# Performance work log

Measured on AMD Instinct MI355X. Metric: run time of the kernel, lower is better.

Reference implementation:

```python
import jax, jax.numpy as jnp
import numpy as np
import math

D_MODEL = 1024
N_HEADS = 16
HEAD_DIM = D_MODEL // N_HEADS
B, T = 2, 2048


def _rope(q, k):
    # q, k: (B, H, T, Dh)
    Dh = q.shape[-1]
    Tq = q.shape[2]
    dim = jnp.arange(0, Dh, 2, dtype=jnp.float32)
    inv_freq = 1.0 / (10000.0 ** (dim / Dh))
    pos = jnp.arange(Tq, dtype=jnp.float32)
    freqs = pos[:, None] * inv_freq[None, :]          # (T, Dh/2)
    sin = jnp.sin(freqs)[None, None]                  # (1,1,T,Dh/2)
    cos = jnp.cos(freqs)[None, None]

    def rot(t):
        te, to = t[..., ::2], t[..., 1::2]
        re = te * cos - to * sin
        ro = te * sin + to * cos
        return jnp.stack([re, ro], axis=-1).reshape(t.shape)

    return rot(q), rot(k)


def setup_inputs() -> dict:
    key = jax.random.key(0)
    ks = jax.random.split(key, 4)
    std = 1.0 / math.sqrt(D_MODEL)
    x = jax.random.normal(ks[0], (B, T, D_MODEL), dtype=jnp.float32)
    W_qkv = jax.random.normal(ks[1], (D_MODEL, 3 * D_MODEL), dtype=jnp.float32) * std
    b_qkv = jnp.zeros((3 * D_MODEL,), dtype=jnp.float32)
    W_out = jax.random.normal(ks[2], (D_MODEL, D_MODEL), dtype=jnp.float32) * std
    b_out = jnp.zeros((D_MODEL,), dtype=jnp.float32)
    attention_mask = jnp.ones((B, T), dtype=jnp.int32)
    return {"x": x, "attention_mask": attention_mask, "W_qkv": W_qkv,
            "b_qkv": b_qkv, "W_out": W_out, "b_out": b_out}


def reference(x, attention_mask, W_qkv, b_qkv, W_out, b_out):
    Bx, Tx, D = x.shape
    qkv = x @ W_qkv + b_qkv                            # (B,T,3D)
    q, k, v = jnp.split(qkv, 3, axis=-1)
    # (B,T,H,Dh) -> (B,H,T,Dh)
    q = q.reshape(Bx, Tx, N_HEADS, HEAD_DIM).transpose(0, 2, 1, 3)
    k = k.reshape(Bx, Tx, N_HEADS, HEAD_DIM).transpose(0, 2, 1, 3)
    v = v.reshape(Bx, Tx, N_HEADS, HEAD_DIM).transpose(0, 2, 1, 3)
    q, k = _rope(q, k)
    scale = 1.0 / math.sqrt(float(HEAD_DIM))
    scores = jnp.einsum('bhqd,bhkd->bhqk', q, k) * scale
    causal = jnp.tril(jnp.ones((Tx, Tx), dtype=bool))[None, None]
    pad = attention_mask.astype(bool)[:, None, None, :]
    mask = causal & pad
    scores = jnp.where(mask, scores, -jnp.inf)
    probs = jax.nn.softmax(scores, axis=-1)
    out = jnp.einsum('bhqk,bhkd->bhqd', probs, v)      # (B,H,T,Dh)
    out = out.transpose(0, 2, 1, 3).reshape(Bx, Tx, D)
    return out @ W_out + b_out
```

## Files before the change

kernel.cpp:

```cpp
#include <hip/hip_runtime.h>
#include <math.h>
#include <stdint.h>

#define D_MODEL 1024
#define N_HEADS 16
#define HEAD_DIM 64
#define BATCH 2
#define SEQ 2048
#define TOKENS (BATCH * SEQ)

typedef __attribute__((ext_vector_type(8))) short short8;
typedef __attribute__((ext_vector_type(8))) _Float16 half8;
typedef __attribute__((ext_vector_type(4))) float floatx4;

#define BMFMA(a, b, c) __builtin_amdgcn_mfma_f32_16x16x32_bf16(a, b, c, 0, 0, 0)
#define HMFMA(a, b, c) __builtin_amdgcn_mfma_f32_16x16x32_f16(a, b, c, 0, 0, 0)

__device__ __forceinline__ unsigned short f2bf(float f) {
    uint32_t u = __float_as_uint(f);
    u += 0x7fffu + ((u >> 16) & 1u);
    return (unsigned short)(u >> 16);
}
__device__ __forceinline__ float bf2f(unsigned short h) {
    return __uint_as_float(((uint32_t)h) << 16);
}
__device__ __forceinline__ unsigned short f2h(float f) {
    union { _Float16 h; unsigned short u; } cv;
    cv.h = (_Float16)f;
    return cv.u;
}
__device__ __forceinline__ float h2f(unsigned short u) {
    union { unsigned short u; _Float16 h; } cv;
    cv.u = u;
    return (float)cv.h;
}

#define GLD_LDS16(gp, lp) __builtin_amdgcn_global_load_lds(                 \
    (const __attribute__((address_space(1))) void*)(gp),                    \
    (__attribute__((address_space(3))) void*)(lp), 16, 0, 0)

__global__ __launch_bounds__(256) void split_inputs(
    const float* __restrict__ X, const float* __restrict__ Wqkv,
    const float* __restrict__ Wout, const int* __restrict__ am,
    unsigned short* __restrict__ Axh, unsigned short* __restrict__ Bt,
    unsigned short* __restrict__ Bt2, unsigned long long* __restrict__ mbits,
    float2* __restrict__ tab)
{
    __shared__ float t[32][33];
    const int tid = threadIdx.x;
    const int bid = blockIdx.x;
    if (bid < 2048) {
        const int idx = bid * 2048 + tid * 8;
        const int row = idx >> 10;
        const int c = idx & 1023;
        float4 v0 = *(const float4*)(X + (size_t)row * 1024 + c);
        float4 v1 = *(const float4*)(X + (size_t)row * 1024 + c + 4);
        float f[8] = {v0.x, v0.y, v0.z, v0.w, v1.x, v1.y, v1.z, v1.w};
        uint32_t p[4];
#pragma unroll
        for (int j = 0; j < 4; ++j)
            p[j] = (uint32_t)f2h(f[2 * j]) | ((uint32_t)f2h(f[2 * j + 1]) << 16);
        *(uint4*)(Axh + (size_t)row * 1024 + c) = *(uint4*)p;
    } else if (bid < 5120) {
        const int id = bid - 2048;
        const int n0 = (id % 96) * 32, k0 = (id / 96) * 32;
        const int c = tid & 31, r = tid >> 5;
#pragma unroll
        for (int i = 0; i < 4; ++i)
            t[r + 8 * i][c] = Wqkv[(size_t)(k0 + r + 8 * i) * 3072 + n0 + c];
        __syncthreads();
#pragma unroll
        for (int i = 0; i < 4; ++i) {
            int dn = r + 8 * i;
            Bt[(size_t)(n0 + dn) * 1024 + k0 + c] = f2h(t[c][dn]);
        }
    } else if (bid < 6144) {
        const int id = bid - 5120;
        const int n0 = (id & 31) * 32, k0 = (id >> 5) * 32;
        const int c = tid & 31, r = tid >> 5;
#pragma unroll
        for (int i = 0; i < 4; ++i)
            t[r + 8 * i][c] = Wout[(size_t)(k0 + r + 8 * i) * 1024 + n0 + c];
        __syncthreads();
#pragma unroll
        for (int i = 0; i < 4; ++i) {
            int dn = r + 8 * i;
            Bt2[(size_t)(n0 + dn) * 1024 + k0 + c] = f2h(t[c][dn]);
        }
    } else if (bid == 6144) {
        if (tid < 64) {
            const int* a = am + tid * 64;
            unsigned long long m = 0ull;
            for (int j = 0; j < 64; ++j)
                m |= (unsigned long long)(a[j] != 0 ? 1u : 0u) << j;
            mbits[tid] = m;
        }
    } else {
        const int i = bid - 6145;
#pragma unroll
        for (int e = 0; e < 16; ++e) {
            int idx = i * 4096 + e * 256 + tid;
            int tt = idx >> 5, pr = idx & 31;
            double ex = (double)(2 * pr) / 64.0;
            float inv = (float)exp2(-ex * 13.287712379549449);
            float ang = (float)tt * inv;
            float s, c;
            __sincosf(ang, &s, &c);
            tab[idx] = make_float2(c, s);
        }
    }
}

__global__ __launch_bounds__(256) void gemm_qkv_fused(
    const unsigned short* __restrict__ Axh, const unsigned short* __restrict__ Bt,
    const float* __restrict__ bias, const float2* __restrict__ tab,
    unsigned short* __restrict__ Qh, unsigned short* __restrict__ Kh,
    unsigned short* __restrict__ Vh)
{
    __shared__ __align__(16) unsigned short sA0[4096], sA1[4096];
    __shared__ __align__(16) unsigned short sB0[4096], sB1[4096];

    const int tid = threadIdx.x;
    const int w = tid >> 6, lane = tid & 63;
    const int l15 = lane & 15, quad = lane >> 4;
    const int wm = w >> 1, wn = w & 1;

    const int lin = blockIdx.x;
    const int s = lin & 7;
    const int loc = lin >> 3;
    const int m0 = ((s >> 1) * 8 + loc / 12) * 128;
    const int n0 = ((s & 1) * 12 + loc % 12) * 128;

    const int ch = (lane & 3) ^ ((lane >> 3) & 3);
    const int sw = (quad ^ ((l15 >> 1) & 3)) * 8;

    const unsigned short* aG[2];
    const unsigned short* bG[2];
#pragma unroll
    for (int i = 0; i < 2; ++i) {
        aG[i] = Axh + (size_t)(m0 + (w * 2 + i) * 16 + (lane >> 2)) * 1024 + ch * 8;
        bG[i] = Bt + (size_t)(n0 + (w * 2 + i) * 16 + (lane >> 2)) * 1024 + ch * 8;
    }

    floatx4 acc[4][4];
#pragma unroll
    for (int fm = 0; fm < 4; ++fm)
#pragma unroll
        for (int fn = 0; fn < 4; ++fn) acc[fm][fn] = (floatx4)0.f;

    for (int ks = 0; ks < 16; ++ks) {
        const int ko = ks * 64;
        __syncthreads();
#pragma unroll
        for (int i = 0; i < 2; ++i) {
            GLD_LDS16(aG[i] + ko,      sA0 + (w * 2 + i) * 512);
            GLD_LDS16(aG[i] + ko + 32, sA1 + (w * 2 + i) * 512);
            GLD_LDS16(bG[i] + ko,      sB0 + (w * 2 + i) * 512);
            GLD_LDS16(bG[i] + ko + 32, sB1 + (w * 2 + i) * 512);
        }
        __syncthreads();

        half8 a0[4], a1[4], b0[4], b1[4];
#pragma unroll
        for (int fm = 0; fm < 4; ++fm) {
            const int off = ((wm * 4 + fm) * 16 + l15) * 32 + sw;
            a0[fm] = *(const half8*)&sA0[off];
            a1[fm] = *(const half8*)&sA1[off];
        }
#pragma unroll
        for (int fn = 0; fn < 4; ++fn) {
            const int off = ((wn * 4 + fn) * 16 + l15) * 32 + sw;
            b0[fn] = *(const half8*)&sB0[off];
            b1[fn] = *(const half8*)&sB1[off];
        }
#pragma unroll
        for (int fm = 0; fm < 4; ++fm)
#pragma unroll
            for (int fn = 0; fn < 4; ++fn) {
                floatx4 a = acc[fm][fn];
                a = HMFMA(a0[fm], b0[fn], a);
                a = HMFMA(a1[fm], b1[fn], a);
                acc[fm][fn] = a;
            }
    }

    if (n0 < 2048) {
        const bool isQ = (n0 < 1024);
        unsigned short* dst = isQ ? Qh : Kh;
        const float qs = isQ ? 0.125f : 1.0f;
#pragma unroll
        for (int fm = 0; fm < 4; ++fm)
#pragma unroll
            for (int fn = 0; fn < 4; ++fn) {
                const int col = n0 + (wn * 4 + fn) * 16 + l15;
                const int hcol = col & 1023;
                const int hh = hcol >> 6, d = hcol & 63;
                const int pr = d >> 1;
                const bool odd = (d & 1) != 0;
                const float bv = bias[col];
#pragma unroll
                for (int r = 0; r < 4; ++r) {
                    const int row = m0 + (wm * 4 + fm) * 16 + quad * 4 + r;
                    const int tg = row & 2047, bb = row >> 11;
                    float val = acc[fm][fn][r] + bv;
                    float part = __shfl_xor(val, 1);
                    const float2 cs = tab[tg * 32 + pr];
                    float res = odd ? (part * cs.y + val * cs.x)
                                    : (val * cs.x - part * cs.y);
                    dst[((size_t)(bb * 16 + hh) * SEQ + tg) * 64 + d] =
                        f2h(res * qs);
                }
            }
    } else {
#pragma unroll
        for (int fm = 0; fm < 4; ++fm)
#pragma unroll
            for (int fn = 0; fn < 4; ++fn) {
                const int col = n0 + (wn * 4 + fn) * 16 + l15;
                const int hcol = col & 1023;
                const int hh = hcol >> 6, d = hcol & 63;
                const float bv = bias[col];
                const int row0 = m0 + (wm * 4 + fm) * 16 + quad * 4;
                const int tg0 = row0 & 2047, bb = row0 >> 11;
                uint32_t pk0 = (uint32_t)f2bf(acc[fm][fn][0] + bv)
                             | ((uint32_t)f2bf(acc[fm][fn][1] + bv) << 16);
                uint32_t pk1 = (uint32_t)f2bf(acc[fm][fn][2] + bv)
                             | ((uint32_t)f2bf(acc[fm][fn][3] + bv) << 16);
                *(uint2*)(Vh + ((size_t)(bb * 16 + hh) * 64 + d) * SEQ + tg0) =
                    make_uint2(pk0, pk1);
            }
    }
}

template<int WM, int WN, int FM, int FN>
__global__ __launch_bounds__(256) void gemm_mfma_h(
    const unsigned short* __restrict__ A, int lda,
    const unsigned short* __restrict__ Bt, int ldb,
    const float* __restrict__ bias, float* __restrict__ C, int ldc,
    int mPerSlab, int nTilesN)
{
    constexpr int BM = WM * FM * 16;
    constexpr int BN = WN * FN * 16;
    constexpr int NA = BM / 64;
    constexpr int NB = BN / 64;

    __shared__ __align__(16) unsigned short sA0[BM * 32];
    __shared__ __align__(16) unsigned short sA1[BM * 32];
    __shared__ __align__(16) unsigned short sB0[BN * 32];
    __shared__ __align__(16) unsigned short sB1[BN * 32];

    const int tid = threadIdx.x;
    const int w = tid >> 6, lane = tid & 63;
    const int l15 = lane & 15, quad = lane >> 4;
    const int wm = w / WN, wn = w % WN;

    const int lin = blockIdx.x;
    const int s = lin & 7, loc = lin >> 3;
    const int m0 = (s * mPerSlab + loc / nTilesN) * BM;
    const int n0 = (loc % nTilesN) * BN;

    const int ch = (lane & 3) ^ ((lane >> 3) & 3);
    const int sw = (quad ^ ((l15 >> 1) & 3)) * 8;

    const unsigned short* aG[NA];
    const unsigned short* bG[NB];
#pragma unroll
    for (int i = 0; i < NA; ++i)
        aG[i] = A + (size_t)(m0 + (w * NA + i) * 16 + (lane >> 2)) * lda + ch * 8;
#pragma unroll
    for (int i = 0; i < NB; ++i)
        bG[i] = Bt + (size_t)(n0 + (w * NB + i) * 16 + (lane >> 2)) * ldb + ch * 8;

    floatx4 acc[FM][FN];
#pragma unroll
    for (int fm = 0; fm < FM; ++fm)
#pragma unroll
        for (int fn = 0; fn < FN; ++fn) acc[fm][fn] = (floatx4)0.f;

    for (int ks = 0; ks < 16; ++ks) {
        const int ko = ks * 64;
        __syncthreads();
#pragma unroll
        for (int i = 0; i < NA; ++i) {
            GLD_LDS16(aG[i] + ko,      sA0 + (w * NA + i) * 512);
            GLD_LDS16(aG[i] + ko + 32, sA1 + (w * NA + i) * 512);
        }
#pragma unroll
        for (int i = 0; i < NB; ++i) {
            GLD_LDS16(bG[i] + ko,      sB0 + (w * NB + i) * 512);
            GLD_LDS16(bG[i] + ko + 32, sB1 + (w * NB + i) * 512);
        }
        __syncthreads();

        half8 a0[FM], a1[FM], b0[FN], b1[FN];
#pragma unroll
        for (int fm = 0; fm < FM; ++fm) {
            const int off = ((wm * FM + fm) * 16 + l15) * 32 + sw;
            a0[fm] = *(const half8*)&sA0[off];
            a1[fm] = *(const half8*)&sA1[off];
        }
#pragma unroll
        for (int fn = 0; fn < FN; ++fn) {
            const int off = ((wn * FN + fn) * 16 + l15) * 32 + sw;
            b0[fn] = *(const half8*)&sB0[off];
            b1[fn] = *(const half8*)&sB1[off];
        }
#pragma unroll
        for (int fm = 0; fm < FM; ++fm)
#pragma unroll
            for (int fn = 0; fn < FN; ++fn) {
                floatx4 a = acc[fm][fn];
                a = HMFMA(a0[fm], b0[fn], a);
                a = HMFMA(a1[fm], b1[fn], a);
                acc[fm][fn] = a;
            }
    }

#pragma unroll
    for (int fm = 0; fm < FM; ++fm)
#pragma unroll
        for (int fn = 0; fn < FN; ++fn) {
            int col = n0 + (wn * FN + fn) * 16 + l15;
            float bv = bias[col];
#pragma unroll
            for (int r = 0; r < 4; ++r) {
                int row = m0 + (wm * FM + fm) * 16 + quad * 4 + r;
                C[(size_t)row * ldc + col] = acc[fm][fn][r] + bv;
            }
        }
}

__global__ __launch_bounds__(256, 6) void flash_mfma(
    const unsigned short* __restrict__ Qh, const unsigned short* __restrict__ Kh,
    const unsigned short* __restrict__ Vh,
    const unsigned long long* __restrict__ mbits,
    unsigned short* __restrict__ attnx,
    float* __restrict__ Opart, float* __restrict__ lpart)
{
    __shared__ __align__(16) unsigned short sK[4096];
    __shared__ __align__(16) unsigned short sV[4096];
    __shared__ __align__(16) unsigned short sP[4096];

    const int tid = threadIdx.x;
    const int lane = tid & 63, w = tid >> 6;
    const int l15 = lane & 15, quad = lane >> 4;
    const int lin0 = blockIdx.x;
    const int xcd = lin0 & 7, idx = lin0 >> 3;
    const int bh = xcd * 4 + (idx & 3);
    const int rank = idx >> 2;
    int qt, k0, kend, mode;
    if (rank < 16)        { qt = 16 + rank; k0 = 0;  kend = 15; mode = 1; }
    else {
        const int i = (rank - 16) >> 1;
        if ((rank & 1) == 0) { qt = 31 - i; k0 = 16; kend = qt; mode = 2; }
        else                 { qt = 15 - i; k0 = 0;  kend = qt; mode = 0; }
    }
    const int b = bh >> 4, h = bh & 15;
    const int sw = (quad ^ ((l15 >> 1) & 3)) * 8;
    const int ch = (lane & 3) ^ ((lane >> 3) & 3);
    unsigned short* pbase = sP + w * 1024;

    short8 ones;
#pragma unroll
    for (int jj = 0; jj < 8; ++jj) ones[jj] = (short)0x3F80;

    const size_t qb = ((size_t)bh * SEQ + qt * 64 + w * 16 + l15) * 64 + quad * 8;
    const half8 qh0 = *(const half8*)(Qh + qb);
    const half8 qh1 = *(const half8*)(Qh + qb + 32);

    unsigned int mlo = 0xffffffffu, mhi = 0xffffffffu;
    if (lane < 32) {
        unsigned long long mw = mbits[b * 32 + lane];
        mlo = (unsigned int)mw;
        mhi = (unsigned int)(mw >> 32);
    }
    const bool fullmask =
        (__ballot((mlo & mhi) == 0xffffffffu) == ~0ull);

    const size_t kRow0 = ((size_t)bh * SEQ + w * 16 + (lane >> 2)) * 64 + ch * 8;
    const size_t vRow  = ((size_t)bh * 64 + w * 16 + (lane >> 2)) * SEQ + ch * 8;

    floatx4 O[4];
    floatx4 lAcc = (floatx4)0.f;
#pragma unroll
    for (int nf = 0; nf < 4; ++nf) O[nf] = (floatx4)0.f;

    const int mg = qt * 64 + w * 16 + l15;

    for (int kt = k0; kt <= kend; ++kt) {
        __syncthreads();
        {
            const size_t kg = kRow0 + (size_t)kt * 64 * 64;
            const size_t vg = vRow + (size_t)kt * 64;
            GLD_LDS16(Kh + kg,      sK + w * 512);
            GLD_LDS16(Kh + kg + 32, sK + 2048 + w * 512);
            GLD_LDS16(Vh + vg,      sV + w * 512);
            GLD_LDS16(Vh + vg + 32, sV + 2048 + w * 512);
        }
        __syncthreads();

        const bool diag = (kt == qt);
        unsigned int wlo = 0xffffffffu, whi = 0xffffffffu;
        if (!fullmask) {
            wlo = (unsigned int)__shfl((int)mlo, kt);
            whi = (unsigned int)__shfl((int)mhi, kt);
        }

#pragma unroll
        for (int nf = 0; nf < 4; ++nf) {
            const int base = (nf * 16 + l15) * 32 + sw;
            const half8 k0v = *(const half8*)&sK[base];
            const half8 k1v = *(const half8*)&sK[2048 + base];
            floatx4 s = (floatx4)0.f;
            s = HMFMA(k0v, qh0, s);
            s = HMFMA(k1v, qh1, s);

            float pv[4];
            if (fullmask && !diag) {
#pragma unroll
                for (int r = 0; r < 4; ++r)
                    pv[r] = __expf(s[r] - 16.0f);
            } else {
                const int tb = kt * 64 + nf * 16 + quad * 4;
                const unsigned int msel = (nf & 2) ? whi : wlo;
                const int p4 = (nf & 1) * 16 + quad * 4;
#pragma unroll
                for (int r = 0; r < 4; ++r) {
                    bool ok = ((msel >> (p4 + r)) & 1u) != 0u;
                    if (diag) ok = ok && (tb + r <= mg);
                    pv[r] = ok ? __expf(s[r] - 16.0f) : 0.0f;
                }
            }
            uint32_t w0, w1;
            asm("v_cvt_pk_bf16_f32 %0, %1, %2" : "=v"(w0) : "v"(pv[0]), "v"(pv[1]));
            asm("v_cvt_pk_bf16_f32 %0, %1, %2" : "=v"(w1) : "v"(pv[2]), "v"(pv[3]));
            const int pos = (((nf & 1) * 2 + (quad >> 1)) ^ ((l15 >> 1) & 3));
            *(uint2*)(pbase + (nf >> 1) * 512 + l15 * 32 + pos * 8
                      + (quad & 1) * 4) = make_uint2(w0, w1);
        }

        const short8 pf0 = *(const short8*)(pbase + l15 * 32 + sw);
        const short8 pf1 = *(const short8*)(pbase + 512 + l15 * 32 + sw);

        lAcc = BMFMA(pf0, ones, lAcc);
        lAcc = BMFMA(pf1, ones, lAcc);
#pragma unroll
        for (int nf = 0; nf < 4; ++nf) {
            const int vb = (nf * 16 + l15) * 32 + sw;
            floatx4 o = O[nf];
            o = BMFMA(pf0, *(const short8*)&sV[vb], o);
            o = BMFMA(pf1, *(const short8*)&sV[2048 + vb], o);
            O[nf] = o;
        }
    }

    if (mode == 0) {
        float rl[4];
#pragma unroll
        for (int r = 0; r < 4; ++r) rl[r] = 1.0f / lAcc[r];
#pragma unroll
        for (int nf = 0; nf < 4; ++nf)
#pragma unroll
            for (int r = 0; r < 4; ++r) {
                const int tok = b * SEQ + qt * 64 + w * 16 + quad * 4 + r;
                const int col = h * 64 + nf * 16 + l15;
                attnx[(size_t)tok * 1024 + col] = f2h(O[nf][r] * rl[r]);
            }
    } else {
        const int qt16 = qt - 16;
        float* Op = Opart + ((mode == 2) ? 2097152 : 0)
                  + (((size_t)bh * 16 + qt16) * 64) * 64;
#pragma unroll
        for (int nf = 0; nf < 4; ++nf)
#pragma unroll
            for (int r = 0; r < 4; ++r)
                Op[(w * 16 + quad * 4 + r) * 64 + nf * 16 + l15] = O[nf][r];
        if (l15 == 0) {
            float* lp = lpart + ((mode == 2) ? 32768 : 0)
                      + (bh * 16 + qt16) * 64;
#pragma unroll
            for (int r = 0; r < 4; ++r)
                lp[w * 16 + quad * 4 + r] = lAcc[r];
        }
    }
}

__global__ __launch_bounds__(256) void flash_merge(
    const float* __restrict__ Opart, const float* __restrict__ lpart,
    unsigned short* __restrict__ attnx)
{
    const int bh = blockIdx.x >> 4, qt16 = blockIdx.x & 15;
    const int b = bh >> 4, h = bh & 15;
    const int tid = threadIdx.x;
    const int q = tid >> 2, dblk = (tid & 3) * 16;
    const size_t ob = (((size_t)bh * 16 + qt16) * 64 + q) * 64 + dblk;
    const int lb = (bh * 16 + qt16) * 64 + q;
    const float rl = 1.0f / (lpart[lb] + lpart[lb + 32768]);

    uint32_t ph[8];
#pragma unroll
    for (int i = 0; i < 4; ++i) {
        float4 a = *(const float4*)(Opart + ob + 4 * i);
        float4 c = *(const float4*)(Opart + ob + 2097152 + 4 * i);
        float f0 = (a.x + c.x) * rl, f1 = (a.y + c.y) * rl;
        float f2 = (a.z + c.z) * rl, f3 = (a.w + c.w) * rl;
        ph[2 * i]     = (uint32_t)f2h(f0) | ((uint32_t)f2h(f1) << 16);
        ph[2 * i + 1] = (uint32_t)f2h(f2) | ((uint32_t)f2h(f3) << 16);
    }
    const int tok = b * SEQ + (16 + qt16) * 64 + q;
    unsigned short* dst = attnx + (size_t)tok * 1024 + h * 64 + dblk;
    *(uint4*)dst = *(uint4*)&ph[0];
    *(uint4*)(dst + 8) = *(uint4*)&ph[4];
}

extern "C" void kernel_launch(void* const* d_in, const int* in_sizes, int n_in,
                              void* d_out, int out_size, void* d_ws, size_t ws_size,
                              hipStream_t stream)
{
    const float* x    = (const float*)d_in[0];
    const int*   am   = (const int*)d_in[1];
    const float* Wqkv = (const float*)d_in[2];
    const float* bqkv = (const float*)d_in[3];
    const float* Wout = (const float*)d_in[4];
    const float* bout = (const float*)d_in[5];
    float* out = (float*)d_out;

    char* ws = (char*)d_ws;
    unsigned short* Bt  = (unsigned short*)ws;
    unsigned short* Bt2 = (unsigned short*)(ws + 6291456);
    float2* tab = (float2*)(ws + 8388608);
    unsigned long long* mbits = (unsigned long long*)(ws + 8912896);
    unsigned short* attnx = (unsigned short*)(ws + 12582912);
    unsigned short* Qh = (unsigned short*)(ws + 62914560);
    unsigned short* Kh = (unsigned short*)(ws + 71303168);
    unsigned short* Vh = (unsigned short*)(ws + 79691776);
    unsigned short* Axh = (unsigned short*)(ws + 88080384);
    float* Opart = (float*)(ws + 88080384);
    float* lpart = (float*)(ws + 104857600);

    split_inputs<<<6161, 256, 0, stream>>>(x, Wqkv, Wout, am,
                                           Axh, Bt, Bt2, mbits, tab);

    gemm_qkv_fused<<<768, 256, 0, stream>>>(Axh, Bt, bqkv, tab, Qh, Kh, Vh);

    flash_mfma<<<1536, 256, 0, stream>>>(Qh, Kh, Vh, mbits, attnx,
                                         Opart, lpart);
    flash_merge<<<512, 256, 0, stream>>>(Opart, lpart, attnx);

    gemm_mfma_h<2, 2, 4, 4><<<256, 256, 0, stream>>>(
        attnx, 1024, Bt2, 1024, bout, out, 1024, 4, 8);
}
```

Before: 184.0 us.

## Double-buffer LDS tiles in QKV and output GEMMs to overlap loads with MFMA

```diff
diff --git a/kernel.cpp b/kernel.cpp
--- a/kernel.cpp
+++ b/kernel.cpp
@@ -38,6 +38,12 @@
 #define GLD_LDS16(gp, lp) __builtin_amdgcn_global_load_lds(                 \
     (const __attribute__((address_space(1))) void*)(gp),                    \
     (__attribute__((address_space(3))) void*)(lp), 16, 0, 0)
+
+#define PIPE_WAIT_BARRIER() do {                                            \
+    asm volatile("s_waitcnt vmcnt(0)" ::: "memory");                        \
+    __builtin_amdgcn_s_barrier();                                           \
+    __builtin_amdgcn_sched_barrier(0);                                      \
+} while (0)
 
 __global__ __launch_bounds__(256) void split_inputs(
     const float* __restrict__ X, const float* __restrict__ Wqkv,
@@ -117,8 +123,8 @@
     unsigned short* __restrict__ Qh, unsigned short* __restrict__ Kh,
     unsigned short* __restrict__ Vh)
 {
-    __shared__ __align__(16) unsigned short sA0[4096], sA1[4096];
-    __shared__ __align__(16) unsigned short sB0[4096], sB1[4096];
+    __shared__ __align__(16) unsigned short sA[2][4096];
+    __shared__ __align__(16) unsigned short sB[2][4096];
 
     const int tid = threadIdx.x;
     const int w = tid >> 6, lane = tid & 63;
@@ -148,40 +154,40 @@
 #pragma unroll
         for (int fn = 0; fn < 4; ++fn) acc[fm][fn] = (floatx4)0.f;
 
-    for (int ks = 0; ks < 16; ++ks) {
-        const int ko = ks * 64;
-        __syncthreads();
-#pragma unroll
-        for (int i = 0; i < 2; ++i) {
-            GLD_LDS16(aG[i] + ko,      sA0 + (w * 2 + i) * 512);
-            GLD_LDS16(aG[i] + ko + 32, sA1 + (w * 2 + i) * 512);
-            GLD_LDS16(bG[i] + ko,      sB0 + (w * 2 + i) * 512);
-            GLD_LDS16(bG[i] + ko + 32, sB1 + (w * 2 + i) * 512);
-        }
-        __syncthreads();
-
-        half8 a0[4], a1[4], b0[4], b1[4];
-#pragma unroll
-        for (int fm = 0; fm < 4; ++fm) {
-            const int off = ((wm * 4 + fm) * 16 + l15) * 32 + sw;
-            a0[fm] = *(const half8*)&sA0[off];
-            a1[fm] = *(const half8*)&sA1[off];
-        }
-#pragma unroll
-        for (int fn = 0; fn < 4; ++fn) {
-            const int off = ((wn * 4 + fn) * 16 + l15) * 32 + sw;
-            b0[fn] = *(const half8*)&sB0[off];
-            b1[fn] = *(const half8*)&sB1[off];
-        }
+#pragma unroll
+    for (int i = 0; i < 2; ++i) {
+        GLD_LDS16(aG[i], &sA[0][(w * 2 + i) * 512]);
+        GLD_LDS16(bG[i], &sB[0][(w * 2 + i) * 512]);
+    }
+    PIPE_WAIT_BARRIER();
+
+    int cur = 0;
+    for (int ks = 0; ks < 32; ++ks) {
+        if (ks < 31) {
+            const int ko = (ks + 1) * 32;
+#pragma unroll
+            for (int i = 0; i < 2; ++i) {
+                GLD_LDS16(aG[i] + ko, &sA[cur ^ 1][(w * 2 + i) * 512]);
+                GLD_LDS16(bG[i] + ko, &sB[cur ^ 1][(w * 2 + i) * 512]);
+            }
+        }
+        __builtin_amdgcn_sched_barrier(0);
+
+        half8 af[4], bf[4];
 #pragma unroll
         for (int fm = 0; fm < 4; ++fm)
-#pragma unroll
-            for (int fn = 0; fn < 4; ++fn) {
-                floatx4 a = acc[fm][fn];
-                a = HMFMA(a0[fm], b0[fn], a);
-                a = HMFMA(a1[fm], b1[fn], a);
-                acc[fm][fn] = a;
-            }
+            af[fm] = *(const half8*)&sA[cur][((wm * 4 + fm) * 16 + l15) * 32 + sw];
+#pragma unroll
+        for (int fn = 0; fn < 4; ++fn)
+            bf[fn] = *(const half8*)&sB[cur][((wn * 4 + fn) * 16 + l15) * 32 + sw];
+#pragma unroll
+        for (int fm = 0; fm < 4; ++fm)
+#pragma unroll
+            for (int fn = 0; fn < 4; ++fn)
+                acc[fm][fn] = HMFMA(af[fm], bf[fn], acc[fm][fn]);
+
+        PIPE_WAIT_BARRIER();
+        cur ^= 1;
     }
 
     if (n0 < 2048) {
@@ -244,10 +250,8 @@
     constexpr int NA = BM / 64;
     constexpr int NB = BN / 64;
 
-    __shared__ __align__(16) unsigned short sA0[BM * 32];
-    __shared__ __align__(16) unsigned short sA1[BM * 32];
-    __shared__ __align__(16) unsigned short sB0[BN * 32];
-    __shared__ __align__(16) unsigned short sB1[BN * 32];
+    __shared__ __align__(16) unsigned short sA[2][BM * 32];
+    __shared__ __align__(16) unsigned short sB[2][BN * 32];
 
     const int tid = threadIdx.x;
     const int w = tid >> 6, lane = tid & 63;
@@ -277,43 +281,42 @@
 #pragma unroll
         for (int fn = 0; fn < FN; ++fn) acc[fm][fn] = (floatx4)0.f;
 
-    for (int ks = 0; ks < 16; ++ks) {
-        const int ko = ks * 64;
-        __syncthreads();
-#pragma unroll
-        for (int i = 0; i < NA; ++i) {
-            GLD_LDS16(aG[i] + ko,      sA0 + (w * NA + i) * 512);
-            GLD_LDS16(aG[i] + ko + 32, sA1 + (w * NA + i) * 512);
-        }
-#pragma unroll
-        for (int i = 0; i < NB; ++i) {
-            GLD_LDS16(bG[i] + ko,      sB0 + (w * NB + i) * 512);
-            GLD_LDS16(bG[i] + ko + 32, sB1 + (w * NB + i) * 512);
-        }
-        __syncthreads();
-
-        half8 a0[FM], a1[FM], b0[FN], b1[FN];
-#pragma unroll
-        for (int fm = 0; fm < FM; ++fm) {
-            const int off = ((wm * FM + fm) * 16 + l15) * 32 + sw;
-            a0[fm] = *(const half8*)&sA0[off];
-            a1[fm] = *(const half8*)&sA1[off];
-        }
-#pragma unroll
-        for (int fn = 0; fn < FN; ++fn) {
-            const int off = ((wn * FN + fn) * 16 + l15) * 32 + sw;
-            b0[fn] = *(const half8*)&sB0[off];
-            b1[fn] = *(const half8*)&sB1[off];
-        }
+#pragma unroll
+    for (int i = 0; i < NA; ++i)
+        GLD_LDS16(aG[i], &sA[0][(w * NA + i) * 512]);
+#pragma unroll
+    for (int i = 0; i < NB; ++i)
+        GLD_LDS16(bG[i], &sB[0][(w * NB + i) * 512]);
+    PIPE_WAIT_BARRIER();
+
+    int cur = 0;
+    for (int ks = 0; ks < 32; ++ks) {
+        if (ks < 31) {
+            const int ko = (ks + 1) * 32;
+#pragma unroll
+            for (int i = 0; i < NA; ++i)
+                GLD_LDS16(aG[i] + ko, &sA[cur ^ 1][(w * NA + i) * 512]);
+#pragma unroll
+            for (int i = 0; i < NB; ++i)
+                GLD_LDS16(bG[i] + ko, &sB[cur ^ 1][(w * NB + i) * 512]);
+        }
+        __builtin_amdgcn_sched_barrier(0);
+
+        half8 af[FM], bf[FN];
 #pragma unroll
         for (int fm = 0; fm < FM; ++fm)
-#pragma unroll
-            for (int fn = 0; fn < FN; ++fn) {
-                floatx4 a = acc[fm][fn];
-                a = HMFMA(a0[fm], b0[fn], a);
-                a = HMFMA(a1[fm], b1[fn], a);
-                acc[fm][fn] = a;
-            }
+            af[fm] = *(const half8*)&sA[cur][((wm * FM + fm) * 16 + l15) * 32 + sw];
+#pragma unroll
+        for (int fn = 0; fn < FN; ++fn)
+            bf[fn] = *(const half8*)&sB[cur][((wn * FN + fn) * 16 + l15) * 32 + sw];
+#pragma unroll
+        for (int fm = 0; fm < FM; ++fm)
+#pragma unroll
+            for (int fn = 0; fn < FN; ++fn)
+                acc[fm][fn] = HMFMA(af[fm], bf[fn], acc[fm][fn]);
+
+        PIPE_WAIT_BARRIER();
+        cur ^= 1;
     }
 
 #pragma unroll
```

Result: slower. 203.6 us (+10.6%).
